# Kernel tuning notes

Measured on AMD Instinct MI355X. Metric: run time of the kernel, lower is better.

Reference implementation:

```python
import math
import jax, jax.numpy as jnp
import numpy as np

# ---- module hyperparameters (from init_kwargs) ----
D = 3            # input_dim
L = 16           # num_levels
C = 2            # level_dim
H = 16           # base_resolution
PS = 2.0         # per_level_scale
LOG2T = 19       # log2_hashmap_size
MAXP = 2 ** LOG2T
HASH_ENTRIES = 4920

# fast_hash primes used by the Instant-NGP / torch-ngp grid encoder (D=3)
PRIME1 = np.uint32(2654435761)
PRIME2 = np.uint32(805459861)


def _make_offsets():
    offsets = [0]
    off = 0
    for i in range(L):
        res = int(math.ceil(H * PS ** i))
        p = min(MAXP, (res + 1) ** D)  # align_corners=False -> res+1 per dim
        p = int(math.ceil(p / 8) * 8)
        off += p
        offsets.append(off)
    return offsets

OFFSETS = _make_offsets()  # [0, 4920, 40864, 315496, ..., 7131240]
TOTAL = OFFSETS[-1]        # 7131240

# corner bit patterns for 2^D trilinear corners, shape [8, 3]
CORNERS = np.array([[(c >> d) & 1 for d in range(D)] for c in range(2 ** D)],
                   dtype=np.uint32)


def setup_inputs() -> dict:
    key = jax.random.key(0)
    k1, k2, k3 = jax.random.split(key, 3)
    std = 1e-4
    inputs = jax.random.uniform(k1, (2097152, D), dtype=jnp.float32)  # in [0,1)
    embeddings = jax.random.uniform(k2, (HASH_ENTRIES, C), jnp.float32,
                                    minval=-std, maxval=std)
    table = jax.random.uniform(k3, (TOTAL - HASH_ENTRIES, C), jnp.float32,
                               minval=-std, maxval=std)
    return {"inputs": inputs, "embeddings": embeddings, "table": table,
            "bound": 1}


def _encode(x01, full_table):
    """x01: [B,3] in [0,1]; full_table: [TOTAL, C] -> [B, L*C]."""
    corners_u = jnp.asarray(CORNERS)                 # [8,3] uint32
    corners_b = jnp.asarray(CORNERS.astype(bool))    # [8,3] bool
    outs = []
    for lvl in range(L):
        scale = H * PS ** lvl - 1.0                  # exp2(l*S)*H - 1
        res = int(math.ceil(scale)) + 1
        hsz = OFFSETS[lvl + 1] - OFFSETS[lvl]
        pos = x01 * jnp.float32(scale) + jnp.float32(0.5)  # align_corners=False
        pg_f = jnp.floor(pos)
        frac = pos - pg_f                            # [B,3]
        pg = pg_f.astype(jnp.uint32)                 # [B,3]
        cg = pg[:, None, :] + corners_u[None]        # [B,8,3]
        # trilinear corner weights
        w = jnp.prod(jnp.where(corners_b[None], frac[:, None, :],
                               1.0 - frac[:, None, :]), axis=-1)  # [B,8]
        if (res + 1) ** D > hsz:
            # hashed level: xor of coord*prime (uint32 wraparound)
            idx = cg[..., 0] ^ (cg[..., 1] * PRIME1) ^ (cg[..., 2] * PRIME2)
        else:
            # dense level: row-major with stride res+1 (align_corners=False)
            s = np.uint32(res + 1)
            idx = cg[..., 0] + cg[..., 1] * s + cg[..., 2] * (s * s)
        idx = (idx % np.uint32(hsz)).astype(jnp.int32) + OFFSETS[lvl]  # [B,8]
        emb = full_table[idx]                        # [B,8,C] gather
        outs.append(jnp.sum(w[..., None] * emb, axis=1))  # [B,C]
    # [L,B,C] permuted to [B, L*C] == concat over levels on last axis
    return jnp.concatenate(outs, axis=-1)


def reference(inputs, embeddings, table, bound):
    full = jnp.concatenate([embeddings, table], axis=0)  # [TOTAL, C]
    x01 = (inputs + bound) / (2 * bound)
    return _encode(x01, full)
```

## Files before the change

### kernel.cpp

```cpp
#include <hip/hip_runtime.h>
#include <cstdint>


static constexpr uint32_t PRIME1 = 2654435761u;
static constexpr uint32_t PRIME2 = 805459861u;
static constexpr uint32_t HASH_MASK = (1u << 19) - 1u;

__constant__ uint32_t c_offs[16] = {
    0u, 4920u, 40864u, 315496u, 839784u, 1364072u, 1888360u, 2412648u,
    2936936u, 3461224u, 3985512u, 4509800u, 5034088u, 5558376u,
    6082664u, 6606952u};

__global__ __launch_bounds__(256) void gather_kernel(
    const float* __restrict__ inputs,
    const float* __restrict__ embeddings,
    const float* __restrict__ table,
    float2* __restrict__ dst,
    int B, int chunks, int directOut)
{
    const int j   = blockIdx.x;
    const int xcd = j & 7;
    const int s   = j >> 3;
    const int lvl = 2 * xcd + (s >= chunks ? 1 : 0);
    const int chunk = (s >= chunks) ? (s - chunks) : s;
    const int base  = chunk * 1024;
    const int tid   = threadIdx.x;

    __shared__ float sIn[3072];
    {
        const float* gp = inputs + (size_t)base * 3;
        const int lim = B * 3 - base * 3;
#pragma unroll
        for (int k = 0; k < 12; ++k) {
            const int i = tid + k * 256;
            if (i < lim) sIn[i] = gp[i];
        }
    }
    __syncthreads();

    const float scale = (float)((16u << lvl) - 1u);
    const uint32_t off = c_offs[lvl];
    const float2* __restrict__ tb = (lvl == 0)
        ? (const float2*)embeddings
        : ((const float2*)table) + (off - 4920u);
    const bool dense = (lvl < 3);
    const uint32_t dstr  = (16u << lvl) + 1u;
    const uint32_t dstr2 = dstr * dstr;

    uint32_t idx[4][8];
    float wts[4][8];

#pragma unroll
    for (int p = 0; p < 4; ++p) {
        const int li = p * 256 + tid;
        const float x01 = __fadd_rn(sIn[li * 3 + 0], 1.0f) * 0.5f;
        const float y01 = __fadd_rn(sIn[li * 3 + 1], 1.0f) * 0.5f;
        const float z01 = __fadd_rn(sIn[li * 3 + 2], 1.0f) * 0.5f;

        const float px = __fadd_rn(__fmul_rn(x01, scale), 0.5f);
        const float py = __fadd_rn(__fmul_rn(y01, scale), 0.5f);
        const float pz = __fadd_rn(__fmul_rn(z01, scale), 0.5f);

        const float fxf = floorf(px), fyf = floorf(py), fzf = floorf(pz);
        const float tx = px - fxf, ty = py - fyf, tz = pz - fzf;
        const uint32_t ix = (uint32_t)fxf, iy = (uint32_t)fyf, iz = (uint32_t)fzf;
        const float wx0 = 1.0f - tx, wy0 = 1.0f - ty, wz0 = 1.0f - tz;

        if (dense) {
            const uint32_t oy0 = iy * dstr,  oy1 = oy0 + dstr;
            const uint32_t oz0 = iz * dstr2, oz1 = oz0 + dstr2;
            idx[p][0] = ix + oy0 + oz0;  idx[p][1] = idx[p][0] + 1u;
            idx[p][2] = ix + oy1 + oz0;  idx[p][3] = idx[p][2] + 1u;
            idx[p][4] = ix + oy0 + oz1;  idx[p][5] = idx[p][4] + 1u;
            idx[p][6] = ix + oy1 + oz1;  idx[p][7] = idx[p][6] + 1u;
        } else {
            const uint32_t hy0 = iy * PRIME1, hy1 = hy0 + PRIME1;
            const uint32_t hz0 = iz * PRIME2, hz1 = hz0 + PRIME2;
            const uint32_t a00 = hy0 ^ hz0, a10 = hy1 ^ hz0;
            const uint32_t a01 = hy0 ^ hz1, a11 = hy1 ^ hz1;
            idx[p][0] = (ix ^ a00) & HASH_MASK;  idx[p][1] = ((ix + 1u) ^ a00) & HASH_MASK;
            idx[p][2] = (ix ^ a10) & HASH_MASK;  idx[p][3] = ((ix + 1u) ^ a10) & HASH_MASK;
            idx[p][4] = (ix ^ a01) & HASH_MASK;  idx[p][5] = ((ix + 1u) ^ a01) & HASH_MASK;
            idx[p][6] = (ix ^ a11) & HASH_MASK;  idx[p][7] = ((ix + 1u) ^ a11) & HASH_MASK;
        }

        const float wxy00 = __fmul_rn(wx0, wy0), wxy10 = __fmul_rn(tx, wy0);
        const float wxy01 = __fmul_rn(wx0, ty),  wxy11 = __fmul_rn(tx, ty);
        wts[p][0] = __fmul_rn(wxy00, wz0); wts[p][1] = __fmul_rn(wxy10, wz0);
        wts[p][2] = __fmul_rn(wxy01, wz0); wts[p][3] = __fmul_rn(wxy11, wz0);
        wts[p][4] = __fmul_rn(wxy00, tz);  wts[p][5] = __fmul_rn(wxy10, tz);
        wts[p][6] = __fmul_rn(wxy01, tz);  wts[p][7] = __fmul_rn(wxy11, tz);
    }

    float2 e[4][8];
#pragma unroll
    for (int p = 0; p < 4; ++p)
#pragma unroll
        for (int c = 0; c < 8; ++c)
            e[p][c] = tb[idx[p][c]];

#pragma unroll
    for (int p = 0; p < 4; ++p) {
        const int b = base + p * 256 + tid;
        if (b >= B) continue;
        float r0 = __fmul_rn(wts[p][0], e[p][0].x);
        float r1 = __fmul_rn(wts[p][0], e[p][0].y);
#pragma unroll
        for (int c = 1; c < 8; ++c) {
            r0 = fmaf(wts[p][c], e[p][c].x, r0);
            r1 = fmaf(wts[p][c], e[p][c].y, r1);
        }
        if (directOut) {
            dst[(size_t)b * 16 + lvl] = make_float2(r0, r1);
        } else {
            dst[(size_t)lvl * B + b] = make_float2(r0, r1);
        }
    }
}

__global__ __launch_bounds__(256) void transpose_kernel(
    const float2* __restrict__ ws, float* __restrict__ out, int B)
{
    __shared__ float sT[256 * 34];
    const int tid = threadIdx.x;
    const int b0  = blockIdx.x * 256;

#pragma unroll
    for (int l = 0; l < 16; ++l) {
        const int b = b0 + tid;
        float2 v = make_float2(0.f, 0.f);
        if (b < B) v = ws[(size_t)l * B + b];
        sT[tid * 34 + 2 * l]     = v.x;
        sT[tid * 34 + 2 * l + 1] = v.y;
    }
    __syncthreads();

    float2* orow = (float2*)(out + (size_t)b0 * 32);
    const int lim = (B - b0) * 16;
#pragma unroll
    for (int it = 0; it < 16; ++it) {
        const int f = it * 256 + tid;
        if (f < lim) {
            const int p = f >> 4;
            const int c = (f & 15) * 2;
            orow[f] = make_float2(sT[p * 34 + c], sT[p * 34 + c + 1]);
        }
    }
}

extern "C" void kernel_launch(void* const* d_in, const int* in_sizes, int n_in,
                              void* d_out, int out_size, void* d_ws, size_t ws_size,
                              hipStream_t stream) {
    const float* inputs     = (const float*)d_in[0];
    const float* embeddings = (const float*)d_in[1];
    const float* table      = (const float*)d_in[2];
    float* out              = (float*)d_out;

    const int B = in_sizes[0] / 3;
    const int chunks = (B + 1023) / 1024;
    const size_t need = (size_t)16 * (size_t)B * sizeof(float2);
    const bool staged = ws_size >= need;

    gather_kernel<<<16 * chunks, 256, 0, stream>>>(
        inputs, embeddings, table,
        staged ? (float2*)d_ws : (float2*)d_out,
        B, chunks, staged ? 0 : 1);

    if (staged) {
        transpose_kernel<<<(B + 255) / 256, 256, 0, stream>>>(
            (const float2*)d_ws, out, B);
    }
}
```

Measured before the change: 1.293 ms.

## Defer weight computation past gathers and vectorize swizzled transpose

The gather kernel now keeps only the three fractional coordinates per point and rebuilds the eight trilinear weights after the table loads. A sched_barrier stops the compiler from moving that arithmetic back ahead of the gathers. This is meant to lower register pressure while the 32 loads are in flight. The transpose kernel is reworked to handle 128 points per block with float4 global loads and stores and an XOR-swizzled shared-memory layout, aiming for wider memory transactions and fewer bank conflicts. The added swizzle indexing logic is more complex and brings some risk at the partial tail block.

```diff
diff --git a/kernel.cpp b/kernel.cpp
--- a/kernel.cpp
+++ b/kernel.cpp
@@ -33,7 +33,7 @@
 #pragma unroll
         for (int k = 0; k < 12; ++k) {
             const int i = tid + k * 256;
-            if (i < lim) sIn[i] = gp[i];
+            sIn[i] = (i < lim) ? gp[i] : 0.0f;
         }
     }
     __syncthreads();
@@ -48,7 +48,7 @@
     const uint32_t dstr2 = dstr * dstr;
 
     uint32_t idx[4][8];
-    float wts[4][8];
+    float fx[4], fy[4], fz[4];
 
 #pragma unroll
     for (int p = 0; p < 4; ++p) {
@@ -62,9 +62,8 @@
         const float pz = __fadd_rn(__fmul_rn(z01, scale), 0.5f);
 
         const float fxf = floorf(px), fyf = floorf(py), fzf = floorf(pz);
-        const float tx = px - fxf, ty = py - fyf, tz = pz - fzf;
+        fx[p] = px - fxf;  fy[p] = py - fyf;  fz[p] = pz - fzf;
         const uint32_t ix = (uint32_t)fxf, iy = (uint32_t)fyf, iz = (uint32_t)fzf;
-        const float wx0 = 1.0f - tx, wy0 = 1.0f - ty, wz0 = 1.0f - tz;
 
         if (dense) {
             const uint32_t oy0 = iy * dstr,  oy1 = oy0 + dstr;
@@ -83,13 +82,6 @@
             idx[p][4] = (ix ^ a01) & HASH_MASK;  idx[p][5] = ((ix + 1u) ^ a01) & HASH_MASK;
             idx[p][6] = (ix ^ a11) & HASH_MASK;  idx[p][7] = ((ix + 1u) ^ a11) & HASH_MASK;
         }
-
-        const float wxy00 = __fmul_rn(wx0, wy0), wxy10 = __fmul_rn(tx, wy0);
-        const float wxy01 = __fmul_rn(wx0, ty),  wxy11 = __fmul_rn(tx, ty);
-        wts[p][0] = __fmul_rn(wxy00, wz0); wts[p][1] = __fmul_rn(wxy10, wz0);
-        wts[p][2] = __fmul_rn(wxy01, wz0); wts[p][3] = __fmul_rn(wxy11, wz0);
-        wts[p][4] = __fmul_rn(wxy00, tz);  wts[p][5] = __fmul_rn(wxy10, tz);
-        wts[p][6] = __fmul_rn(wxy01, tz);  wts[p][7] = __fmul_rn(wxy11, tz);
     }
 
     float2 e[4][8];
@@ -98,17 +90,28 @@
 #pragma unroll
         for (int c = 0; c < 8; ++c)
             e[p][c] = tb[idx[p][c]];
+    __builtin_amdgcn_sched_barrier(0);
 
 #pragma unroll
     for (int p = 0; p < 4; ++p) {
         const int b = base + p * 256 + tid;
         if (b >= B) continue;
-        float r0 = __fmul_rn(wts[p][0], e[p][0].x);
-        float r1 = __fmul_rn(wts[p][0], e[p][0].y);
+        const float tx = fx[p], ty = fy[p], tz = fz[p];
+        const float wx0 = 1.0f - tx, wy0 = 1.0f - ty, wz0 = 1.0f - tz;
+        const float wxy00 = __fmul_rn(wx0, wy0), wxy10 = __fmul_rn(tx, wy0);
+        const float wxy01 = __fmul_rn(wx0, ty),  wxy11 = __fmul_rn(tx, ty);
+        float w[8];
+        w[0] = __fmul_rn(wxy00, wz0); w[1] = __fmul_rn(wxy10, wz0);
+        w[2] = __fmul_rn(wxy01, wz0); w[3] = __fmul_rn(wxy11, wz0);
+        w[4] = __fmul_rn(wxy00, tz);  w[5] = __fmul_rn(wxy10, tz);
+        w[6] = __fmul_rn(wxy01, tz);  w[7] = __fmul_rn(wxy11, tz);
+
+        float r0 = __fmul_rn(w[0], e[p][0].x);
+        float r1 = __fmul_rn(w[0], e[p][0].y);
 #pragma unroll
         for (int c = 1; c < 8; ++c) {
-            r0 = fmaf(wts[p][c], e[p][c].x, r0);
-            r1 = fmaf(wts[p][c], e[p][c].y, r1);
+            r0 = fmaf(w[c], e[p][c].x, r0);
+            r1 = fmaf(w[c], e[p][c].y, r1);
         }
         if (directOut) {
             dst[(size_t)b * 16 + lvl] = make_float2(r0, r1);
@@ -121,30 +124,42 @@
 __global__ __launch_bounds__(256) void transpose_kernel(
     const float2* __restrict__ ws, float* __restrict__ out, int B)
 {
-    __shared__ float sT[256 * 34];
+    __shared__ float sT[128 * 36];
     const int tid = threadIdx.x;
-    const int b0  = blockIdx.x * 256;
+    const int b0  = blockIdx.x * 128;
+    const bool full = (b0 + 128 <= B);
 
 #pragma unroll
-    for (int l = 0; l < 16; ++l) {
-        const int b = b0 + tid;
-        float2 v = make_float2(0.f, 0.f);
-        if (b < B) v = ws[(size_t)l * B + b];
-        sT[tid * 34 + 2 * l]     = v.x;
-        sT[tid * 34 + 2 * l + 1] = v.y;
+    for (int k = 0; k < 4; ++k) {
+        const int idx = k * 256 + tid;
+        const int l   = idx >> 6;
+        const int q   = idx & 63;
+        const int b   = b0 + 2 * q;
+        float4 v = make_float4(0.f, 0.f, 0.f, 0.f);
+        if (full) {
+            v = *(const float4*)(&ws[(size_t)l * B + b]);
+        } else {
+            if (b < B)     { float2 t = ws[(size_t)l * B + b];     v.x = t.x; v.y = t.y; }
+            if (b + 1 < B) { float2 t = ws[(size_t)l * B + b + 1]; v.z = t.x; v.w = t.y; }
+        }
+        const int c2 = l ^ (q & 15);
+        *(float2*)&sT[(2 * q)     * 36 + 2 * c2] = make_float2(v.x, v.y);
+        *(float2*)&sT[(2 * q + 1) * 36 + 2 * c2] = make_float2(v.z, v.w);
     }
     __syncthreads();
 
-    float2* orow = (float2*)(out + (size_t)b0 * 32);
-    const int lim = (B - b0) * 16;
+    float4* orow = (float4*)(out + (size_t)b0 * 32);
+    const int lim4 = (B - b0) * 8;
 #pragma unroll
-    for (int it = 0; it < 16; ++it) {
-        const int f = it * 256 + tid;
-        if (f < lim) {
-            const int p = f >> 4;
-            const int c = (f & 15) * 2;
-            orow[f] = make_float2(sT[p * 34 + c], sT[p * 34 + c + 1]);
-        }
+    for (int k = 0; k < 4; ++k) {
+        const int f = k * 256 + tid;
+        if (f >= lim4) continue;
+        const int p = f >> 3;
+        const int jj = f & 7;
+        const int q = p >> 1;
+        const int y = (2 * jj) ^ (q & 15);
+        const float4 v = *(const float4*)&sT[p * 36 + 2 * (y & ~1)];
+        orow[f] = (q & 1) ? make_float4(v.z, v.w, v.x, v.y) : v;
     }
 }
 
@@ -167,7 +182,7 @@
         B, chunks, staged ? 0 : 1);
 
     if (staged) {
-        transpose_kernel<<<(B + 255) / 256, 256, 0, stream>>>(
+        transpose_kernel<<<(B + 127) / 128, 256, 0, stream>>>(
             (const float2*)d_ws, out, B);
     }
 }
```

After: 1.267 ms. -2.0%, faster.
